# Optimization experiments

Hardware: AMD Instinct MI355X
Metric: run time of the kernel (lower is better)

The kernel has to match this reference:

```python
import jax, jax.numpy as jnp
import numpy as np

N = 2708
IN_C = 1433
OUT_C = 64


def setup_inputs() -> dict:
    key = jax.random.key(0)
    k1, k2, k3, k4, k5, k6, k7 = jax.random.split(key, 7)
    X = jax.random.normal(k1, (N, IN_C), dtype=jnp.float32)
    A = jax.random.randint(k2, (N, N), 0, 2, dtype=jnp.int32)  # dense binary adjacency mask
    # Graph Fourier basis: orthonormal-ish random matrix (QR of gaussian)
    U = jnp.linalg.qr(jax.random.normal(k3, (N, N), dtype=jnp.float32))[0]
    s = 1.0 / np.sqrt(IN_C)
    W_K = jax.random.normal(k4, (OUT_C, IN_C), dtype=jnp.float32) * s
    W_Q = jax.random.normal(k5, (OUT_C, IN_C), dtype=jnp.float32) * s
    W_V = jax.random.normal(k6, (OUT_C, IN_C), dtype=jnp.float32) * s
    lmbd = jax.random.uniform(k7, (N, 1), dtype=jnp.float32)
    return {"X": X, "A": A, "U": U, "W_K": W_K, "W_Q": W_Q, "W_V": W_V, "lmbd": lmbd}


def reference(X, A, U, W_K, W_Q, W_V, lmbd):
    # Linear projections (torch nn.Linear: x @ W.T)
    K = X @ W_K.T  # [N, d]
    Q = X @ W_Q.T  # [N, d]
    V = X @ W_V.T  # [N, d]
    d_k = K.shape[-1]
    E = (Q @ K.T) / d_k  # [N, N]
    # spectral filtering: igft(lmbd * gft(E)) = U @ (lmbd * (U^T @ E))
    E = jnp.abs(U @ (lmbd * (U.T @ E)))
    # masked softmax over neighbors; dropout p=0 in eval mode (no-op)
    E_masked = jnp.where(A == 0, -jnp.inf, E)
    alpha = jax.nn.softmax(E_masked, axis=-1)
    H = alpha @ V  # [N, d]
    return H
```

## Files before the change

kernel.cpp:

```cpp
#include <hip/hip_runtime.h>

#define NV 2708
#define INC 1433
#define XCOLS 1472
#define UDIM 2752
#define PSTR 2728
#define BSTR 2752
#define SLAB ((size_t)(2752*64))
#define MWPR 88
#define NSP 4
#define NSU 11

typedef __attribute__((ext_vector_type(8))) short bf16x8;
typedef __attribute__((ext_vector_type(4))) float f32x4;
typedef __attribute__((ext_vector_type(4))) unsigned short u16x4;

__device__ __forceinline__ unsigned short f2bf(float f){
  union { float f; unsigned int i; } v; v.f = f;
  return (unsigned short)((v.i + 0x7fffu + ((v.i >> 16) & 1u)) >> 16);
}

__device__ __forceinline__ void conv_row(const float* __restrict__ src,
                                         unsigned short* __restrict__ dst, int tid){
  const int sh = ((unsigned int)((size_t)src >> 2)) & 1;
  if (tid == 0){ int ce = sh ? 0 : (INC - 1); dst[ce] = f2bf(src[ce]); }
  const float2* s2 = (const float2*)(src + sh);
  for (int c2 = tid; c2 < (INC - 1)/2; c2 += 256){
    float2 v = s2[c2];
    int c = sh + c2*2;
    dst[c]     = f2bf(v.x);
    dst[c + 1] = f2bf(v.y);
  }
  for (int c = INC + tid; c < XCOLS; c += 256) dst[c] = 0;
}

__global__ __launch_bounds__(256) void convert_all(
    const float* __restrict__ X, const float* __restrict__ WK,
    const float* __restrict__ WQ, const float* __restrict__ WV,
    const float* __restrict__ U, const int* __restrict__ A,
    unsigned short* __restrict__ Xbf, unsigned short* __restrict__ Wbf,
    unsigned short* __restrict__ Ubf, unsigned short* __restrict__ UTbf,
    unsigned int* __restrict__ Abits)
{
  __shared__ __align__(16) float tpose[64][68];
  const int bx = blockIdx.x;
  const int tid = threadIdx.x;
  if (bx < 2752){
    const int row = bx;
    unsigned short* dst = Xbf + (size_t)row*XCOLS;
    if (row < NV){
      conv_row(X + (size_t)row*INC, dst, tid);
    } else {
      u16x4 zz = {0,0,0,0};
      for (int c4 = tid; c4 < XCOLS/4; c4 += 256) *(u16x4*)(dst + c4*4) = zz;
    }
  } else if (bx < 2944){
    const int row = bx - 2752;
    const float* s = (row < 64) ? WK : (row < 128) ? WQ : WV;
    conv_row(s + (size_t)(row & 63)*INC, Wbf + (size_t)row*XCOLS, tid);
  } else if (bx < 5652){
    const int i = bx - 2944;
    const int lane = tid & 63, wave = tid >> 6;
    const int* arow = A + (size_t)i*NV;
    unsigned int* drow = Abits + (size_t)i*MWPR;
    for (int g = wave; g < 11; g += 4){
      int base = g*256 + lane*4;
      int4 v = make_int4(0,0,0,0);
      if (base < NV) v = *(const int4*)(arow + base);
      unsigned long long m0 = __ballot(v.x != 0);
      unsigned long long m1 = __ballot(v.y != 0);
      unsigned long long m2 = __ballot(v.z != 0);
      unsigned long long m3 = __ballot(v.w != 0);
      if (lane < 8){
        unsigned long long mm = (lane < 2) ? m0 : (lane < 4) ? m1 : (lane < 6) ? m2 : m3;
        drow[g*8 + lane] = (lane & 1) ? (unsigned int)(mm >> 32) : (unsigned int)mm;
      }
    }
  } else {
    const int t = bx - 5652;
    const int tx = t % 43, ty = t / 43;
    const int r0 = ty*64, c0 = tx*64;
    #pragma unroll
    for (int j = 0; j < 4; j++){
      int row = j*16 + (tid >> 4);
      int c4  = (tid & 15)*4;
      float4 v = make_float4(0.f,0.f,0.f,0.f);
      if (r0 + row < NV && c0 + c4 < NV)
        v = *(const float4*)(U + (size_t)(r0+row)*NV + c0 + c4);
      *(float4*)&tpose[row][c4] = v;
      u16x4 h = { f2bf(v.x), f2bf(v.y), f2bf(v.z), f2bf(v.w) };
      *(u16x4*)(Ubf + (size_t)(r0+row)*UDIM + c0 + c4) = h;
    }
    __syncthreads();
    const int i = tid >> 2;
    #pragma unroll
    for (int j = 0; j < 4; j++){
      int kk = ((tid & 3) + j*4)*4;
      u16x4 h = { f2bf(tpose[kk+0][i]), f2bf(tpose[kk+1][i]),
                  f2bf(tpose[kk+2][i]), f2bf(tpose[kk+3][i]) };
      *(u16x4*)(UTbf + (size_t)(c0+i)*UDIM + r0 + kk) = h;
    }
  }
}

__global__ __launch_bounds__(256) void proj(
    const unsigned short* __restrict__ Xbf, const unsigned short* __restrict__ Wbf,
    float* __restrict__ part)
{
  __shared__ __align__(16) unsigned short At[32*72];
  __shared__ __align__(16) unsigned short Bt[64*72];
  const int tid = threadIdx.x;
  const int lane = tid & 63, wave = tid >> 6, quad = lane >> 4, lr = lane & 15;
  const int m0 = blockIdx.x * 32;
  const int s  = blockIdx.y, z = blockIdx.z;
  const int kbeg = s * 384, kend = min(kbeg + 384, XCOLS);
  const int wm = (wave & 1) * 16, wn = (wave >> 1) * 32;
  const unsigned short* Wz = Wbf + (size_t)z*64*XCOLS;
  const int arow = tid >> 3, aseg = tid & 7;
  const int brow = tid >> 2, bseg = tid & 3;
  f32x4 acc[2] = {};

  for (int k0 = kbeg; k0 < kend; k0 += 64){
    *(bf16x8*)&At[arow*72 + aseg*8] =
        *(const bf16x8*)(Xbf + (size_t)(m0+arow)*XCOLS + k0 + aseg*8);
    {
      const unsigned short* b = Wz + (size_t)brow*XCOLS + k0 + bseg*16;
      *(bf16x8*)&Bt[brow*72 + bseg*16]     = *(const bf16x8*)(b);
      *(bf16x8*)&Bt[brow*72 + bseg*16 + 8] = *(const bf16x8*)(b + 8);
    }
    __syncthreads();
    #pragma unroll
    for (int ks = 0; ks < 2; ks++){
      bf16x8 af = *(const bf16x8*)&At[(wm + lr)*72 + ks*32 + quad*8];
      bf16x8 bv[2];
      #pragma unroll
      for (int t = 0; t < 2; t++)
        bv[t] = *(const bf16x8*)&Bt[(wn + t*16 + lr)*72 + ks*32 + quad*8];
      #pragma unroll
      for (int t = 0; t < 2; t++)
        acc[t] = __builtin_amdgcn_mfma_f32_16x16x32_bf16(af, bv[t], acc[t], 0, 0, 0);
    }
    __syncthreads();
  }
  float* dst = part + (size_t)(z*NSP + s) * SLAB;
  #pragma unroll
  for (int t = 0; t < 2; t++)
    #pragma unroll
    for (int e = 0; e < 4; e++)
      dst[(size_t)(m0 + wm + quad*4 + e)*64 + wn + t*16 + lr] = acc[t][e];
}

__global__ __launch_bounds__(256) void reduce_proj(
    const float* __restrict__ part, unsigned short* __restrict__ K16f,
    unsigned short* __restrict__ QT16, unsigned short* __restrict__ VTf)
{
  int idx = blockIdx.x*256 + threadIdx.x;
  int z = blockIdx.y;
  int m = idx >> 6, c = idx & 63;
  const float* base = part + (size_t)z*NSP*SLAB + idx;
  float v = 0.f;
  #pragma unroll
  for (int s = 0; s < NSP; s++) v += base[s*SLAB];
  unsigned short h = (m < NV) ? f2bf(v) : (unsigned short)0;
  if (z == 0){
    if (m < 2720) K16f[((m>>4)*2 + (c>>5))*512 + (m&15)*32 + (c&31)] = h;
  } else if (z == 1){
    QT16[(size_t)c*BSTR + m] = h;
  } else {
    if (m < 2720) VTf[(m>>5)*2048 + c*32 + (m&31)] = h;
  }
}

__global__ __launch_bounds__(256) void gemmU(
    const unsigned short* __restrict__ Arow, const unsigned short* __restrict__ Bcm,
    float* __restrict__ part)
{
  __shared__ __align__(16) unsigned short At[32*72];
  __shared__ __align__(16) unsigned short Bt[64*72];
  const int tid = threadIdx.x;
  const int lane = tid & 63, wave = tid >> 6, quad = lane >> 4, lr = lane & 15;
  const int m0 = blockIdx.x * 32;
  const int s  = blockIdx.y;
  const int kbeg = s * 256, kend = min(kbeg + 256, UDIM);
  const int wm = (wave & 1) * 16, wn = (wave >> 1) * 32;
  const int arow = tid >> 3, aseg = tid & 7;
  const int bc = tid >> 2, bseg = tid & 3;
  f32x4 acc[2] = {};

  for (int k0 = kbeg; k0 < kend; k0 += 64){
    *(bf16x8*)&At[arow*72 + aseg*8] =
        *(const bf16x8*)(Arow + (size_t)(m0+arow)*UDIM + k0 + aseg*8);
    {
      const unsigned short* b = Bcm + (size_t)bc*BSTR + k0 + bseg*16;
      *(bf16x8*)&Bt[bc*72 + bseg*16]     = *(const bf16x8*)(b);
      *(bf16x8*)&Bt[bc*72 + bseg*16 + 8] = *(const bf16x8*)(b + 8);
    }
    __syncthreads();
    #pragma unroll
    for (int ks = 0; ks < 2; ks++){
      bf16x8 af = *(const bf16x8*)&At[(wm + lr)*72 + ks*32 + quad*8];
      bf16x8 bv[2];
      #pragma unroll
      for (int t = 0; t < 2; t++)
        bv[t] = *(const bf16x8*)&Bt[(wn + t*16 + lr)*72 + ks*32 + quad*8];
      #pragma unroll
      for (int t = 0; t < 2; t++)
        acc[t] = __builtin_amdgcn_mfma_f32_16x16x32_bf16(af, bv[t], acc[t], 0, 0, 0);
    }
    __syncthreads();
  }
  float* dst = part + (size_t)s * SLAB;
  #pragma unroll
  for (int t = 0; t < 2; t++)
    #pragma unroll
    for (int e = 0; e < 4; e++)
      dst[(size_t)(m0 + wm + quad*4 + e)*64 + wn + t*16 + lr] = acc[t][e];
}

__global__ __launch_bounds__(256) void reduce_g(
    const float* __restrict__ part, const float* __restrict__ lm,
    unsigned short* __restrict__ G2T)
{
  int idx = blockIdx.x*256 + threadIdx.x;
  int m = idx >> 6, c = idx & 63;
  const float* base = part + idx;
  float v = 0.f;
  #pragma unroll
  for (int s = 0; s < NSU; s++) v += base[s*SLAB];
  unsigned short h = 0;
  if (m < NV) h = f2bf(v * lm[m] * (1.0f/64.0f));
  G2T[(size_t)c*BSTR + m] = h;
}

__global__ __launch_bounds__(512) void fused_attn(
    const unsigned short* __restrict__ Ubf, const unsigned short* __restrict__ G2T,
    const unsigned short* __restrict__ K16f,
    const unsigned int* __restrict__ Abits, const unsigned short* __restrict__ VTf,
    float* __restrict__ Hout)
{
  __shared__ __align__(16) unsigned short pbuf[16*PSTR];
  __shared__ __align__(16) unsigned short fbuf[16*64];
  __shared__ unsigned int mrow[16*MWPR];
  __shared__ float swave[8][16];
  __shared__ float rinv[16];
  __shared__ __align__(16) float obuf[4][256];
  const int tid  = threadIdx.x;
  const int lane = tid & 63, wave = tid >> 6;
  const int quad = lane >> 4, lr = lane & 15;
  const int i0 = blockIdx.x * 16;

  float* fpart = (float*)pbuf;
  {
    f32x4 facc[4] = {};
    const unsigned short* ua = Ubf + (size_t)(i0 + lr)*UDIM + quad*8;
    for (int ks = wave; ks < 86; ks += 8){
      const int k0 = ks*32;
      bf16x8 af = *(const bf16x8*)(ua + k0);
      #pragma unroll
      for (int n = 0; n < 4; n++){
        bf16x8 bv = *(const bf16x8*)(G2T + (size_t)(n*16 + lr)*BSTR + k0 + quad*8);
        facc[n] = __builtin_amdgcn_mfma_f32_16x16x32_bf16(af, bv, facc[n], 0, 0, 0);
      }
    }
    #pragma unroll
    for (int n = 0; n < 4; n++)
      *(f32x4*)&fpart[(wave*4 + n)*256 + lane*4] = facc[n];
  }
  for (int idx = tid; idx < 16*MWPR; idx += 512){
    int r = idx / MWPR;
    unsigned int v = 0;
    if (i0 + r < NV) v = Abits[(size_t)(i0 + r)*MWPR + (idx - r*MWPR)];
    mrow[idx] = v;
  }
  __syncthreads();
  for (int idx = tid; idx < 1024; idx += 512){
    int n = idx >> 8, l4 = idx & 255;
    float v = 0.f;
    #pragma unroll
    for (int w = 0; w < 8; w++) v += fpart[(w*4 + n)*256 + l4];
    int l = l4 >> 2, e = l4 & 3;
    fbuf[((l >> 4)*4 + e)*64 + n*16 + (l & 15)] = f2bf(v);
  }
  __syncthreads();

  const bf16x8 af0 = *(const bf16x8*)&fbuf[lr*64 + quad*8];
  const bf16x8 af1 = *(const bf16x8*)&fbuf[lr*64 + 32 + quad*8];
  float psum[4] = {0.f, 0.f, 0.f, 0.f};
  {
    int t = wave;
    const unsigned short* kb = K16f + t*1024 + lr*32 + quad*8;
    bf16x8 b0 = *(const bf16x8*)(kb);
    bf16x8 b1 = *(const bf16x8*)(kb + 512);
    while (t < 170){
      int tn = t + 8;
      bf16x8 n0 = b0, n1 = b1;
      if (tn < 170){
        const unsigned short* nb = K16f + tn*1024 + lr*32 + quad*8;
        n0 = *(const bf16x8*)(nb);
        n1 = *(const bf16x8*)(nb + 512);
      }
      f32x4 sv0 = {}, sv1 = {};
      sv0 = __builtin_amdgcn_mfma_f32_16x16x32_bf16(af0, b0, sv0, 0, 0, 0);
      sv1 = __builtin_amdgcn_mfma_f32_16x16x32_bf16(af1, b1, sv1, 0, 0, 0);
      f32x4 sv = sv0 + sv1;
      {
        int col = t*16 + lr;
        int ss = col & 255, ll = ss >> 2;
        int wsh = (col >> 8)*8 + (ss & 3)*2 + (ll >> 5);
        int bit = ll & 31;
        #pragma unroll
        for (int e = 0; e < 4; e++){
          int r = quad*4 + e;
          float p = 0.f;
          if ((mrow[r*MWPR + wsh] >> bit) & 1u) p = __expf(fabsf(sv[e]));
          psum[e] += p;
          pbuf[r*PSTR + col] = f2bf(p);
        }
      }
      b0 = n0; b1 = n1; t = tn;
    }
  }
  #pragma unroll
  for (int e = 0; e < 4; e++){
    float v = psum[e];
    #pragma unroll
    for (int o = 1; o <= 8; o <<= 1) v += __shfl_xor(v, o, 64);
    if (lr == 0) swave[wave][quad*4 + e] = v;
  }
  __syncthreads();
  if (tid < 16){
    float s = 0.f;
    #pragma unroll
    for (int w = 0; w < 8; w++) s += swave[w][tid];
    rinv[tid] = (s > 0.f) ? (1.f/s) : 0.f;
  }
  __syncthreads();

  const int c0 = (wave & 3) * 16;
  const int ktbeg = (wave >> 2) ? 43 : 0;
  const int ktend = (wave >> 2) ? 85 : 43;
  f32x4 acc = {};
  {
    bf16x8 bv = *(const bf16x8*)&VTf[ktbeg*2048 + (c0 + lr)*32 + quad*8];
    for (int kt = ktbeg; kt < ktend; kt++){
      bf16x8 bn = bv;
      if (kt + 1 < ktend) bn = *(const bf16x8*)&VTf[(kt+1)*2048 + (c0 + lr)*32 + quad*8];
      bf16x8 af = *(const bf16x8*)&pbuf[lr*PSTR + kt*32 + quad*8];
      acc = __builtin_amdgcn_mfma_f32_16x16x32_bf16(af, bv, acc, 0, 0, 0);
      bv = bn;
    }
  }
  if (wave >= 4) *(f32x4*)&obuf[wave & 3][lane*4] = acc;
  __syncthreads();
  if (wave < 4){
    f32x4 o = *(const f32x4*)&obuf[wave][lane*4];
    acc += o;
    #pragma unroll
    for (int e = 0; e < 4; e++){
      int r = quad*4 + e;
      int i = i0 + r;
      if (i < NV) Hout[(size_t)i*64 + c0 + lr] = acc[e] * rinv[r];
    }
  }
}

extern "C" void kernel_launch(void* const* d_in, const int* in_sizes, int n_in,
                              void* d_out, int out_size, void* d_ws, size_t ws_size,
                              hipStream_t stream){
  (void)in_sizes; (void)n_in; (void)out_size; (void)ws_size;
  const float* X  = (const float*)d_in[0];
  const int*   A  = (const int*)d_in[1];
  const float* U  = (const float*)d_in[2];
  const float* WK = (const float*)d_in[3];
  const float* WQ = (const float*)d_in[4];
  const float* WV = (const float*)d_in[5];
  const float* lm = (const float*)d_in[6];

  char* ws = (char*)d_ws;
  size_t off = 0;
  auto alloc = [&](size_t bytes){ size_t o = off; off = (off + bytes + 255) & ~(size_t)255; return o; };
  float*          part = (float*)(ws + alloc(12*SLAB*4));
  unsigned short* Ubf  = (unsigned short*)(ws + alloc((size_t)UDIM*UDIM*2));
  unsigned short* UTbf = (unsigned short*)(ws + alloc((size_t)UDIM*UDIM*2));
  unsigned short* Xbf  = (unsigned short*)(ws + alloc((size_t)UDIM*XCOLS*2));
  unsigned short* Wbf  = (unsigned short*)(ws + alloc((size_t)192*XCOLS*2));
  unsigned short* K16f = (unsigned short*)(ws + alloc((size_t)170*1024*2));
  unsigned short* QT16 = (unsigned short*)(ws + alloc((size_t)64*BSTR*2));
  unsigned short* G2T  = (unsigned short*)(ws + alloc((size_t)64*BSTR*2));
  unsigned short* VTf  = (unsigned short*)(ws + alloc((size_t)85*2048*2));
  unsigned int*   Abits= (unsigned int*)(ws + alloc((size_t)NV*MWPR*4));

  convert_all<<<dim3(7501), 256, 0, stream>>>(X, WK, WQ, WV, U, A,
                                              Xbf, Wbf, Ubf, UTbf, Abits);
  proj<<<dim3(86, NSP, 3), 256, 0, stream>>>(Xbf, Wbf, part);
  reduce_proj<<<dim3(688, 3), 256, 0, stream>>>(part, K16f, QT16, VTf);
  gemmU<<<dim3(86, NSU), 256, 0, stream>>>(UTbf, QT16, part);
  reduce_g<<<dim3(688), 256, 0, stream>>>(part, lm, G2T);
  fused_attn<<<dim3(170), 512, 0, stream>>>(Ubf, G2T, K16f, Abits, VTf, (float*)d_out);
}
```

Before: 176.7 us.

## Fuse U fp32-to-bf16 conversion and transpose into consuming GEMM loads

Removes the separate pass that converted U to bf16 and wrote both U and U^T copies. The U^T·Q GEMM now reads fp32 U rows directly and transposes them into shared memory while converting. The attention kernel converts fp32 U rows to bf16 in registers. This saves a full read of U plus two bf16 writes and their later re-reads, but the GEMMs now read twice the bytes per element of U, and the transposed shared-memory stores are scalar and may cause bank conflicts.

```diff
diff --git a/kernel.cpp b/kernel.cpp
--- a/kernel.cpp
+++ b/kernel.cpp
@@ -37,12 +37,10 @@
 __global__ __launch_bounds__(256) void convert_all(
     const float* __restrict__ X, const float* __restrict__ WK,
     const float* __restrict__ WQ, const float* __restrict__ WV,
-    const float* __restrict__ U, const int* __restrict__ A,
+    const int* __restrict__ A,
     unsigned short* __restrict__ Xbf, unsigned short* __restrict__ Wbf,
-    unsigned short* __restrict__ Ubf, unsigned short* __restrict__ UTbf,
     unsigned int* __restrict__ Abits)
 {
-  __shared__ __align__(16) float tpose[64][68];
   const int bx = blockIdx.x;
   const int tid = threadIdx.x;
   if (bx < 2752){
@@ -58,7 +56,7 @@
     const int row = bx - 2752;
     const float* s = (row < 64) ? WK : (row < 128) ? WQ : WV;
     conv_row(s + (size_t)(row & 63)*INC, Wbf + (size_t)row*XCOLS, tid);
-  } else if (bx < 5652){
+  } else {
     const int i = bx - 2944;
     const int lane = tid & 63, wave = tid >> 6;
     const int* arow = A + (size_t)i*NV;
@@ -76,30 +74,6 @@
         drow[g*8 + lane] = (lane & 1) ? (unsigned int)(mm >> 32) : (unsigned int)mm;
       }
     }
-  } else {
-    const int t = bx - 5652;
-    const int tx = t % 43, ty = t / 43;
-    const int r0 = ty*64, c0 = tx*64;
-    #pragma unroll
-    for (int j = 0; j < 4; j++){
-      int row = j*16 + (tid >> 4);
-      int c4  = (tid & 15)*4;
-      float4 v = make_float4(0.f,0.f,0.f,0.f);
-      if (r0 + row < NV && c0 + c4 < NV)
-        v = *(const float4*)(U + (size_t)(r0+row)*NV + c0 + c4);
-      *(float4*)&tpose[row][c4] = v;
-      u16x4 h = { f2bf(v.x), f2bf(v.y), f2bf(v.z), f2bf(v.w) };
-      *(u16x4*)(Ubf + (size_t)(r0+row)*UDIM + c0 + c4) = h;
-    }
-    __syncthreads();
-    const int i = tid >> 2;
-    #pragma unroll
-    for (int j = 0; j < 4; j++){
-      int kk = ((tid & 3) + j*4)*4;
-      u16x4 h = { f2bf(tpose[kk+0][i]), f2bf(tpose[kk+1][i]),
-                  f2bf(tpose[kk+2][i]), f2bf(tpose[kk+3][i]) };
-      *(u16x4*)(UTbf + (size_t)(c0+i)*UDIM + r0 + kk) = h;
-    }
   }
 }
 
@@ -171,8 +145,8 @@
   }
 }
 
-__global__ __launch_bounds__(256) void gemmU(
-    const unsigned short* __restrict__ Arow, const unsigned short* __restrict__ Bcm,
+__global__ __launch_bounds__(256) void gemmG(
+    const float* __restrict__ U, const unsigned short* __restrict__ Bcm,
     float* __restrict__ part)
 {
   __shared__ __align__(16) unsigned short At[32*72];
@@ -183,13 +157,23 @@
   const int s  = blockIdx.y;
   const int kbeg = s * 256, kend = min(kbeg + 256, UDIM);
   const int wm = (wave & 1) * 16, wn = (wave >> 1) * 32;
-  const int arow = tid >> 3, aseg = tid & 7;
+  const int ml = (tid & 7)*4, kr = tid >> 3;
   const int bc = tid >> 2, bseg = tid & 3;
+  const bool mok = (m0 + ml) < NV;
   f32x4 acc[2] = {};
 
   for (int k0 = kbeg; k0 < kend; k0 += 64){
-    *(bf16x8*)&At[arow*72 + aseg*8] =
-        *(const bf16x8*)(Arow + (size_t)(m0+arow)*UDIM + k0 + aseg*8);
+    #pragma unroll
+    for (int e = 0; e < 2; e++){
+      int kl = kr + e*32;
+      int row = k0 + kl;
+      float4 v = make_float4(0.f,0.f,0.f,0.f);
+      if (row < NV && mok) v = *(const float4*)(U + (size_t)row*NV + m0 + ml);
+      At[(ml+0)*72 + kl] = f2bf(v.x);
+      At[(ml+1)*72 + kl] = f2bf(v.y);
+      At[(ml+2)*72 + kl] = f2bf(v.z);
+      At[(ml+3)*72 + kl] = f2bf(v.w);
+    }
     {
       const unsigned short* b = Bcm + (size_t)bc*BSTR + k0 + bseg*16;
       *(bf16x8*)&Bt[bc*72 + bseg*16]     = *(const bf16x8*)(b);
@@ -233,7 +217,7 @@
 }
 
 __global__ __launch_bounds__(512) void fused_attn(
-    const unsigned short* __restrict__ Ubf, const unsigned short* __restrict__ G2T,
+    const float* __restrict__ U, const unsigned short* __restrict__ G2T,
     const unsigned short* __restrict__ K16f,
     const unsigned int* __restrict__ Abits, const unsigned short* __restrict__ VTf,
     float* __restrict__ Hout)
@@ -252,10 +236,29 @@
   float* fpart = (float*)pbuf;
   {
     f32x4 facc[4] = {};
-    const unsigned short* ua = Ubf + (size_t)(i0 + lr)*UDIM + quad*8;
+    const bool rok = (i0 + lr) < NV;
+    const float* urow = U + (size_t)(i0 + lr)*NV;
     for (int ks = wave; ks < 86; ks += 8){
       const int k0 = ks*32;
-      bf16x8 af = *(const bf16x8*)(ua + k0);
+      const int kc = k0 + quad*8;
+      bf16x8 af;
+      if (!rok){
+        #pragma unroll
+        for (int j = 0; j < 8; j++) af[j] = 0;
+      } else if (kc + 7 < NV){
+        float4 a = *(const float4*)(urow + kc);
+        float4 b = *(const float4*)(urow + kc + 4);
+        af[0] = (short)f2bf(a.x); af[1] = (short)f2bf(a.y);
+        af[2] = (short)f2bf(a.z); af[3] = (short)f2bf(a.w);
+        af[4] = (short)f2bf(b.x); af[5] = (short)f2bf(b.y);
+        af[6] = (short)f2bf(b.z); af[7] = (short)f2bf(b.w);
+      } else {
+        #pragma unroll
+        for (int j = 0; j < 8; j++){
+          int col = kc + j;
+          af[j] = (col < NV) ? (short)f2bf(urow[col]) : (short)0;
+        }
+      }
       #pragma unroll
       for (int n = 0; n < 4; n++){
         bf16x8 bv = *(const bf16x8*)(G2T + (size_t)(n*16 + lr)*BSTR + k0 + quad*8);
@@ -380,8 +383,6 @@
   size_t off = 0;
   auto alloc = [&](size_t bytes){ size_t o = off; off = (off + bytes + 255) & ~(size_t)255; return o; };
   float*          part = (float*)(ws + alloc(12*SLAB*4));
-  unsigned short* Ubf  = (unsigned short*)(ws + alloc((size_t)UDIM*UDIM*2));
-  unsigned short* UTbf = (unsigned short*)(ws + alloc((size_t)UDIM*UDIM*2));
   unsigned short* Xbf  = (unsigned short*)(ws + alloc((size_t)UDIM*XCOLS*2));
   unsigned short* Wbf  = (unsigned short*)(ws + alloc((size_t)192*XCOLS*2));
   unsigned short* K16f = (unsigned short*)(ws + alloc((size_t)170*1024*2));
@@ -390,11 +391,10 @@
   unsigned short* VTf  = (unsigned short*)(ws + alloc((size_t)85*2048*2));
   unsigned int*   Abits= (unsigned int*)(ws + alloc((size_t)NV*MWPR*4));
 
-  convert_all<<<dim3(7501), 256, 0, stream>>>(X, WK, WQ, WV, U, A,
-                                              Xbf, Wbf, Ubf, UTbf, Abits);
+  convert_all<<<dim3(5652), 256, 0, stream>>>(X, WK, WQ, WV, A, Xbf, Wbf, Abits);
   proj<<<dim3(86, NSP, 3), 256, 0, stream>>>(Xbf, Wbf, part);
   reduce_proj<<<dim3(688, 3), 256, 0, stream>>>(part, K16f, QT16, VTf);
-  gemmU<<<dim3(86, NSU), 256, 0, stream>>>(UTbf, QT16, part);
+  gemmG<<<dim3(86, NSU), 256, 0, stream>>>(U, QT16, part);
   reduce_g<<<dim3(688), 256, 0, stream>>>(part, lm, G2T);
-  fused_attn<<<dim3(170), 512, 0, stream>>>(Ubf, G2T, K16f, Abits, VTf, (float*)d_out);
-}
+  fused_attn<<<dim3(170), 512, 0, stream>>>(U, G2T, K16f, Abits, VTf, (float*)d_out);
+}
```

Measured after the change: 173.3 us. About the same (-1.9%).
